# Kernel tuning notes

Hardware: AMD Instinct MI355X
Metric: run time of the kernel (lower is better)

Reference implementation:

```python
import jax, jax.numpy as jnp
import numpy as np

N = 262144
B = 16
C = 256
H = 8


def setup_inputs() -> dict:
    key = jax.random.key(0)
    ks = jax.random.split(key, 12)
    s = 0.02
    inp = {
        'x_a': jax.random.normal(ks[0], (N, C), jnp.float32),
        'x_b': jax.random.normal(ks[1], (N, C), jnp.float32),
        'offset': (jnp.arange(1, B + 1, dtype=jnp.int64) * (N // B)),
        'Wq': jax.random.normal(ks[2], (C, C), jnp.float32) * s,
        'Wk': jax.random.normal(ks[3], (C, C), jnp.float32) * s,
        'Wv': jax.random.normal(ks[4], (C, C), jnp.float32) * s,
        'Wp': jax.random.normal(ks[5], (C, C), jnp.float32) * s,
        'bp': jnp.zeros((C,), jnp.float32),
        'Wr1': jax.random.normal(ks[6], (C, C), jnp.float32) * s,
        'br1': jnp.zeros((C,), jnp.float32),
        'Wr2': jax.random.normal(ks[7], (C, C), jnp.float32) * s,
        'br2': jnp.zeros((C,), jnp.float32),
        'gamma': jnp.zeros((1,), jnp.float32),
        'Wo': jax.random.normal(ks[8], (C, C), jnp.float32) * s,
        'bo': jnp.zeros((C,), jnp.float32),
    }
    return inp


def reference(x_a, x_b, offset, Wq, Wk, Wv, Wp, bp, Wr1, br1, Wr2, br2, gamma, Wo, bo):
    n, c = x_a.shape
    b = offset.shape[0]
    h = H
    dh = c // h
    scale = dh ** -0.5
    # segment id for each point (offsets are cumulative counts)
    seg = jnp.searchsorted(offset, jnp.arange(n), side='right')
    counts = (offset - jnp.concatenate([jnp.zeros((1,), offset.dtype), offset[:-1]])).astype(x_a.dtype)
    # per-segment mean pool of branch A -> CLS queries
    cls_a = jax.ops.segment_sum(x_a, seg, num_segments=b) / counts[:, None]
    q = (cls_a @ Wq).reshape(b, h, dh)            # (B,H,Dh)
    k = (x_b @ Wk).reshape(n, h, dh)              # (N,H,Dh)
    v = (x_b @ Wv).reshape(n, h, dh)
    # ragged cross-attention: one query per segment over its own points
    logits = jnp.einsum('nhd,nhd->nh', k, q[seg]) * scale   # (N,H)
    m = jax.lax.stop_gradient(jax.ops.segment_max(logits, seg, num_segments=b))
    p = jnp.exp(logits - m[seg])
    denom = jax.ops.segment_sum(p, seg, num_segments=b)     # (B,H)
    w = p / denom[seg]
    out_cls = jax.ops.segment_sum(w[:, :, None] * v, seg, num_segments=b).reshape(b, c)
    out_cls = out_cls @ Wp + bp                   # proj (dropout = identity at eval)
    cls_proj = jax.nn.relu(out_cls @ Wr1 + br1) @ Wr2 + br2  # reproj MLP
    fused = x_a + gamma * cls_proj[seg]           # broadcast-scatter back to points
    return fused @ Wo + bo
```

## Files before the change

kernel.cpp:

```cpp
#include <hip/hip_runtime.h>


#define NPTS 262144
#define NSEG 16
#define CDIM 256
#define HNUM 8
#define DH   32
#define NB   2048

#define GEMM_BLOCKS 256
#define GEMM_NT     4096

using bf16x8 = __attribute__((ext_vector_type(8))) __bf16;
using f32x16 = __attribute__((ext_vector_type(16))) float;

__device__ __forceinline__ unsigned short f2bf(float f) {
  unsigned int u = __float_as_uint(f);
  unsigned int r = u + 0x7FFFu + ((u >> 16) & 1u);
  return (unsigned short)(r >> 16);
}

__device__ __forceinline__ bool off_is64(const int* o) { return o[1] == 0; }
__device__ __forceinline__ long long off_at(const int* o, int i, bool is64) {
  return is64 ? ((const long long*)o)[i] : (long long)o[i];
}
__device__ __forceinline__ int seg_of(long long row, const int* o, bool is64) {
  int s = 0;
  while (s < NSEG - 1 && row >= off_at(o, s, is64)) ++s;
  return s;
}

template <int CTRL>
__device__ __forceinline__ float dpp_add(float x) {
  int m = __builtin_amdgcn_update_dpp(0, __float_as_int(x), CTRL, 0xF, 0xF, true);
  return x + __int_as_float(m);
}

__device__ __forceinline__ void allred8(float lp[8]) {
  #pragma unroll
  for (int h = 0; h < 8; ++h) {
    float s = lp[h];
    s = dpp_add<0xB1>(s);
    s = dpp_add<0x4E>(s);
    s = dpp_add<0x124>(s);
    s = dpp_add<0x128>(s);
    s += __shfl_xor(s, 16, 64);
    s += __shfl_xor(s, 32, 64);
    lp[h] = s;
  }
}

__global__ __launch_bounds__(256) void k_wotseg(const float* __restrict__ Wo,
                                                unsigned short* __restrict__ wotp,
                                                const float* __restrict__ xa,
                                                const int* __restrict__ off,
                                                float* __restrict__ Apart,
                                                int* __restrict__ taga,
                                                float* __restrict__ cls_atomic,
                                                const float* __restrict__ gamma,
                                                int use_slots) {
  if (blockIdx.x < 256) {
    const int o = blockIdx.x * 256 + threadIdx.x;
    const int k = o >> 8, n = o & 255;
    wotp[n * CDIM + k] = f2bf(Wo[o]);
    return;
  }
  if (*gamma == 0.0f) return;
  const int bid = blockIdx.x - 256;
  const bool is64 = off_is64(off);
  const int t = threadIdx.x, lane = t & 63, w = t >> 6;
  const long long r0b = (long long)bid * 128;
  const int sg0 = seg_of(r0b, off, is64), sg1 = seg_of(r0b + 127, off, is64);
  const long long rw0 = r0b + (long long)w * 32;
  __shared__ float red[4][256];

  if (use_slots && sg0 == sg1) {
    float acc[4] = {0.f, 0.f, 0.f, 0.f};
    for (int r = 0; r < 32; ++r) {
      float4 xv = *(const float4*)&xa[(rw0 + r) * CDIM + lane * 4];
      acc[0] += xv.x; acc[1] += xv.y; acc[2] += xv.z; acc[3] += xv.w;
    }
    *(float4*)&red[w][lane * 4] = make_float4(acc[0], acc[1], acc[2], acc[3]);
    __syncthreads();
    Apart[bid * 256 + t] = red[0][t] + red[1][t] + red[2][t] + red[3][t];
    if (t == 0) taga[bid] = sg0;
  } else {
    int sg = seg_of(rw0, off, is64);
    long long segend = off_at(off, sg, is64);
    float acc[4] = {0.f, 0.f, 0.f, 0.f};
    for (int r = 0; r < 32; ++r) {
      long long row = rw0 + r;
      if (row >= segend) {
        #pragma unroll
        for (int i = 0; i < 4; ++i) { atomicAdd(&cls_atomic[sg * CDIM + lane * 4 + i], acc[i]); acc[i] = 0.f; }
        sg = seg_of(row, off, is64);
        segend = off_at(off, sg, is64);
      }
      float4 xv = *(const float4*)&xa[row * CDIM + lane * 4];
      acc[0] += xv.x; acc[1] += xv.y; acc[2] += xv.z; acc[3] += xv.w;
    }
    #pragma unroll
    for (int i = 0; i < 4; ++i) atomicAdd(&cls_atomic[sg * CDIM + lane * 4 + i], acc[i]);
    if (use_slots) {
      Apart[bid * 256 + t] = 0.f;
      if (t == 0) taga[bid] = -1;
    }
  }
}

__global__ __launch_bounds__(256) void k_prep(const float* __restrict__ Apart,
                                              const int* __restrict__ taga,
                                              const float* __restrict__ cls_atomic,
                                              const int* __restrict__ off,
                                              const float* __restrict__ Wq,
                                              const float* __restrict__ Wk,
                                              float* __restrict__ Kq,
                                              const float* __restrict__ gamma,
                                              int nb) {
  if (*gamma == 0.0f) return;
  const int b = blockIdx.x, t = threadIdx.x;
  const bool is64 = off_is64(off);
  __shared__ float cls[256], qv[256];
  long long lo = b ? off_at(off, b - 1, is64) : 0;
  long long hi = off_at(off, b, is64);
  float s = cls_atomic[b * CDIM + t];
  if (nb > 0) {
    int wlo = (int)(lo / 128); if (wlo < 0) wlo = 0;
    int whi = (int)((hi + 127) / 128); if (whi > nb) whi = nb;
    for (int w = wlo; w < whi; ++w)
      if (taga[w] == b) s += Apart[w * 256 + t];
  }
  cls[t] = s;
  __syncthreads();
  long long cnt = hi - lo; if (cnt < 1) cnt = 1;
  float inv = 1.0f / (float)cnt;
  float qs = 0.f;
  for (int c = 0; c < CDIM; ++c) qs += cls[c] * Wq[c * CDIM + t];
  qv[t] = qs * inv;
  __syncthreads();
  const float scale = 0.17677669529663687f;
  #pragma unroll
  for (int h = 0; h < HNUM; ++h) {
    float kk = 0.f;
    #pragma unroll 8
    for (int d = 0; d < DH; ++d) kk += Wk[t * CDIM + h * DH + d] * qv[h * DH + d];
    Kq[(b * HNUM + h) * CDIM + t] = kk * scale;
  }
}

__global__ __launch_bounds__(256) void k_stats(const float* __restrict__ xb,
                                               const int* __restrict__ off,
                                               const float* __restrict__ Kq,
                                               float* __restrict__ Spart,
                                               float* __restrict__ Dpart,
                                               int* __restrict__ tags,
                                               float* __restrict__ S_atomic,
                                               float* __restrict__ denom_atomic,
                                               const float* __restrict__ gamma,
                                               int use_slots) {
  if (*gamma == 0.0f) return;
  const bool is64 = off_is64(off);
  const int t = threadIdx.x, lane = t & 63, w = t >> 6;
  const long long r0b = (long long)blockIdx.x * 128;
  const int sg0 = seg_of(r0b, off, is64), sg1 = seg_of(r0b + 127, off, is64);
  const long long rw0 = r0b + (long long)w * 32;
  __shared__ float red[4][2048];
  __shared__ float dred[4][8];

  if (use_slots && sg0 == sg1) {
    float kq[8][4];
    #pragma unroll
    for (int h = 0; h < 8; ++h) {
      float4 v = *(const float4*)&Kq[(sg0 * 8 + h) * CDIM + lane * 4];
      kq[h][0] = v.x; kq[h][1] = v.y; kq[h][2] = v.z; kq[h][3] = v.w;
    }
    float sacc[8][4]; float dacc[8];
    #pragma unroll
    for (int h = 0; h < 8; ++h) { dacc[h] = 0.f; sacc[h][0]=sacc[h][1]=sacc[h][2]=sacc[h][3]=0.f; }

    #pragma unroll 2
    for (int r = 0; r < 32; ++r) {
      float4 xv = *(const float4*)&xb[(rw0 + r) * CDIM + lane * 4];
      float lp[8];
      #pragma unroll
      for (int h = 0; h < 8; ++h)
        lp[h] = xv.x*kq[h][0] + xv.y*kq[h][1] + xv.z*kq[h][2] + xv.w*kq[h][3];
      allred8(lp);
      #pragma unroll
      for (int h = 0; h < 8; ++h) {
        float p = __expf(lp[h]);
        dacc[h] += p;
        sacc[h][0] += p*xv.x; sacc[h][1] += p*xv.y; sacc[h][2] += p*xv.z; sacc[h][3] += p*xv.w;
      }
    }
    #pragma unroll
    for (int h = 0; h < 8; ++h)
      *(float4*)&red[w][h * 256 + lane * 4] = make_float4(sacc[h][0], sacc[h][1], sacc[h][2], sacc[h][3]);
    if (lane == 0) {
      #pragma unroll
      for (int h = 0; h < 8; ++h) dred[w][h] = dacc[h];
    }
    __syncthreads();
    #pragma unroll
    for (int k = 0; k < 8; ++k) {
      int e = k * 256 + t;
      Spart[(long long)blockIdx.x * 2048 + e] = red[0][e] + red[1][e] + red[2][e] + red[3][e];
    }
    if (t < 8) Dpart[blockIdx.x * 8 + t] = dred[0][t] + dred[1][t] + dred[2][t] + dred[3][t];
    if (t == 0) tags[blockIdx.x] = sg0;
  } else {
    int sg = seg_of(rw0, off, is64);
    long long segend = off_at(off, sg, is64);
    float kq[8][4];
    #pragma unroll
    for (int h = 0; h < 8; ++h) {
      float4 v = *(const float4*)&Kq[(sg * 8 + h) * CDIM + lane * 4];
      kq[h][0] = v.x; kq[h][1] = v.y; kq[h][2] = v.z; kq[h][3] = v.w;
    }
    float sacc[8][4]; float dacc[8];
    #pragma unroll
    for (int h = 0; h < 8; ++h) { dacc[h] = 0.f; sacc[h][0]=sacc[h][1]=sacc[h][2]=sacc[h][3]=0.f; }
    for (int r = 0; r < 32; ++r) {
      long long row = rw0 + r;
      if (row >= segend) {
        #pragma unroll
        for (int h = 0; h < 8; ++h) {
          #pragma unroll
          for (int i = 0; i < 4; ++i) { atomicAdd(&S_atomic[(sg*8+h)*CDIM + lane*4 + i], sacc[h][i]); sacc[h][i]=0.f; }
          if (lane == 0) atomicAdd(&denom_atomic[sg*8+h], dacc[h]);
          dacc[h] = 0.f;
        }
        sg = seg_of(row, off, is64);
        segend = off_at(off, sg, is64);
        #pragma unroll
        for (int h = 0; h < 8; ++h) {
          float4 v = *(const float4*)&Kq[(sg * 8 + h) * CDIM + lane * 4];
          kq[h][0] = v.x; kq[h][1] = v.y; kq[h][2] = v.z; kq[h][3] = v.w;
        }
      }
      float4 xv = *(const float4*)&xb[row * CDIM + lane * 4];
      float lp[8];
      #pragma unroll
      for (int h = 0; h < 8; ++h)
        lp[h] = xv.x*kq[h][0] + xv.y*kq[h][1] + xv.z*kq[h][2] + xv.w*kq[h][3];
      allred8(lp);
      #pragma unroll
      for (int h = 0; h < 8; ++h) {
        float p = __expf(lp[h]);
        dacc[h] += p;
        sacc[h][0] += p*xv.x; sacc[h][1] += p*xv.y; sacc[h][2] += p*xv.z; sacc[h][3] += p*xv.w;
      }
    }
    #pragma unroll
    for (int h = 0; h < 8; ++h) {
      #pragma unroll
      for (int i = 0; i < 4; ++i) atomicAdd(&S_atomic[(sg*8+h)*CDIM + lane*4 + i], sacc[h][i]);
      if (lane == 0) atomicAdd(&denom_atomic[sg*8+h], dacc[h]);
    }
    if (use_slots) {
      #pragma unroll
      for (int k = 0; k < 8; ++k) Spart[(long long)blockIdx.x * 2048 + k * 256 + t] = 0.f;
      if (t < 8) Dpart[blockIdx.x * 8 + t] = 0.f;
      if (t == 0) tags[blockIdx.x] = -1;
    }
  }
}

__global__ __launch_bounds__(256) void k_sred(const float* __restrict__ Spart,
                                              const float* __restrict__ Dpart,
                                              const int* __restrict__ tags,
                                              const float* __restrict__ S_atomic,
                                              const float* __restrict__ denom_atomic,
                                              const int* __restrict__ off,
                                              float* __restrict__ S,
                                              float* __restrict__ denom,
                                              const float* __restrict__ gamma,
                                              int nb) {
  if (*gamma == 0.0f) return;
  const int b = blockIdx.x >> 3, ch = blockIdx.x & 7, t = threadIdx.x;
  const bool is64 = off_is64(off);
  const int e = ch * 256 + t;
  long long lo = b ? off_at(off, b - 1, is64) : 0;
  long long hi = off_at(off, b, is64);
  int wlo = (int)(lo / 128); if (wlo < 0) wlo = 0;
  int whi = (int)((hi + 127) / 128); if (whi > nb) whi = nb;
  float s = S_atomic[b * 2048 + e];
  for (int w = wlo; w < whi; ++w)
    if (tags[w] == b) s += Spart[(long long)w * 2048 + e];
  S[b * 2048 + e] = s;
  if (ch == 0 && t < 8) {
    float d = denom_atomic[b * 8 + t];
    for (int w = wlo; w < whi; ++w)
      if (tags[w] == b) d += Dpart[w * 8 + t];
    denom[b * 8 + t] = d;
  }
}

__global__ __launch_bounds__(256) void k_post(const float* __restrict__ S,
                                              const float* __restrict__ denom,
                                              const float* __restrict__ Wv,
                                              const float* __restrict__ Wp, const float* __restrict__ bp,
                                              const float* __restrict__ Wr1, const float* __restrict__ br1,
                                              const float* __restrict__ Wr2, const float* __restrict__ br2,
                                              const float* __restrict__ gamma,
                                              const float* __restrict__ Wo, const float* __restrict__ bo,
                                              float* __restrict__ biasv) {
  const int b = blockIdx.x, t = threadIdx.x;
  const float g = *gamma;
  if (g == 0.0f) {
    biasv[b * CDIM + t] = bo[t];
    return;
  }
  __shared__ float sb[8][256];
  __shared__ float db[8];
  __shared__ float v0[256], v1[256];
  #pragma unroll
  for (int k = 0; k < 8; ++k) sb[k][t] = S[b * 2048 + k * 256 + t];
  if (t < 8) db[t] = denom[b * 8 + t];
  __syncthreads();
  const int h = t >> 5;
  float oc = 0.f;
  for (int c = 0; c < CDIM; ++c) oc += Wv[c * CDIM + t] * sb[h][c];
  oc /= db[h];
  v0[t] = oc;
  __syncthreads();
  float a = bp[t];
  for (int c = 0; c < CDIM; ++c) a += v0[c] * Wp[c * CDIM + t];
  v1[t] = a;
  __syncthreads();
  float r1 = br1[t];
  for (int c = 0; c < CDIM; ++c) r1 += v1[c] * Wr1[c * CDIM + t];
  r1 = fmaxf(r1, 0.f);
  v0[t] = r1;
  __syncthreads();
  float r2 = br2[t];
  for (int c = 0; c < CDIM; ++c) r2 += v0[c] * Wr2[c * CDIM + t];
  v1[t] = r2;
  __syncthreads();
  float acc = 0.f;
  for (int c = 0; c < CDIM; ++c) acc += v1[c] * Wo[c * CDIM + t];
  biasv[b * CDIM + t] = bo[t] + g * acc;
}

__device__ __forceinline__ void gemm_mfma_step(const unsigned short* Abuf,
                                               const unsigned short* Bs,
                                               int rA, int hi16, int nB0, int nB1, int sbyte,
                                               f32x16& acc0, f32x16& acc1) {
  #pragma unroll
  for (int ks = 0; ks < 4; ++ks) {
    const bf16x8 a = *(const bf16x8*)((const char*)Abuf + rA * 128 +
                       ((ks * 32 + hi16) ^ ((rA & 7) << 4)));
    const bf16x8 b0 = *(const bf16x8*)((const char*)Bs + nB0 * 512 +
                       ((sbyte + ks * 32 + hi16) ^ ((nB0 & 31) << 4)));
    const bf16x8 b1 = *(const bf16x8*)((const char*)Bs + nB1 * 512 +
                       ((sbyte + ks * 32 + hi16) ^ ((nB1 & 31) << 4)));
    acc0 = __builtin_amdgcn_mfma_f32_32x32x16_bf16(a, b0, acc0, 0, 0, 0);
    acc1 = __builtin_amdgcn_mfma_f32_32x32x16_bf16(a, b1, acc1, 0, 0, 0);
  }
}

__device__ __forceinline__ void gemm_cvt_write(const float4& sa, const float4& sb,
                                               unsigned short* Abuf, int aws0, int aws1) {
  unsigned int u0 = (unsigned int)f2bf(sa.x) | ((unsigned int)f2bf(sa.y) << 16);
  unsigned int u1 = (unsigned int)f2bf(sa.z) | ((unsigned int)f2bf(sa.w) << 16);
  unsigned int u2 = (unsigned int)f2bf(sb.x) | ((unsigned int)f2bf(sb.y) << 16);
  unsigned int u3 = (unsigned int)f2bf(sb.z) | ((unsigned int)f2bf(sb.w) << 16);
  uint2 w0; w0.x = u0; w0.y = u1;
  uint2 w1; w1.x = u2; w1.y = u3;
  *(uint2*)((char*)Abuf + aws0) = w0;
  *(uint2*)((char*)Abuf + aws1) = w1;
}

#define GEMM_BAR() do { asm volatile("s_waitcnt lgkmcnt(0)" ::: "memory"); \
                        __builtin_amdgcn_s_barrier(); } while (0)

#define GEMM_TILE(TCUR, PNEXT, c0,c1,c2,c3,c4,c5,c6,c7, n0,n1,n2,n3,n4,n5,n6,n7)   \
  {                                                                                 \
    f32x16 acc0 = {}, acc1 = {};                                                    \
    const long long r0 = (TCUR) * 64;                                               \
    gemm_cvt_write(c0, c1, As0, aws0, aws1);                                        \
    n0 = *(const float4*)(PNEXT);       n1 = *(const float4*)((PNEXT) + 32 * CDIM); \
    GEMM_BAR();                                                                     \
    gemm_mfma_step(As0, Bs, rA, hi16, nB0, nB1, 0, acc0, acc1);                     \
    gemm_cvt_write(c2, c3, As1, aws0, aws1);                                        \
    n2 = *(const float4*)((PNEXT) + 64); n3 = *(const float4*)((PNEXT) + 64 + 32 * CDIM); \
    GEMM_BAR();                                                                     \
    gemm_mfma_step(As1, Bs, rA, hi16, nB0, nB1, 128, acc0, acc1);                   \
    gemm_cvt_write(c4, c5, As0, aws0, aws1);                                        \
    n4 = *(const float4*)((PNEXT) + 128); n5 = *(const float4*)((PNEXT) + 128 + 32 * CDIM); \
    GEMM_BAR();                                                                     \
    gemm_mfma_step(As0, Bs, rA, hi16, nB0, nB1, 256, acc0, acc1);                   \
    gemm_cvt_write(c6, c7, As1, aws0, aws1);                                        \
    n6 = *(const float4*)((PNEXT) + 192); n7 = *(const float4*)((PNEXT) + 192 + 32 * CDIM); \
    GEMM_BAR();                                                                     \
    gemm_mfma_step(As1, Bs, rA, hi16, nB0, nB1, 384, acc0, acc1);                   \
    const int sg0 = seg_of(r0, off, is64);                                          \
    const bool uni = (sg0 == seg_of(r0 + 63, off, is64));                           \
    const int col0 = wx * 64 + (lane & 31);                                         \
    const int col1 = col0 + 32;                                                     \
    const float bvu0 = bias[sg0 * CDIM + col0];                                     \
    const float bvu1 = bias[sg0 * CDIM + col1];                                     \
    _Pragma("unroll")                                                               \
    for (int reg = 0; reg < 16; ++reg) {                                            \
      const int rin = wy * 32 + 4 * (lane >> 5) + (reg & 3) + 8 * (reg >> 2);       \
      const long long grow = r0 + rin;                                              \
      float bb0 = bvu0, bb1 = bvu1;                                                 \
      if (!uni) {                                                                   \
        const int sg = seg_of(grow, off, is64);                                     \
        bb0 = bias[sg * CDIM + col0];                                               \
        bb1 = bias[sg * CDIM + col1];                                               \
      }                                                                             \
      out[grow * CDIM + col0] = acc0[reg] + bb0;                                    \
      out[grow * CDIM + col1] = acc1[reg] + bb1;                                    \
    }                                                                               \
  }

__global__ __launch_bounds__(512, 2) void k_gemm(const float* __restrict__ xa,
                                                 const unsigned short* __restrict__ wot,
                                                 const float* __restrict__ bias,
                                                 const int* __restrict__ off,
                                                 float* __restrict__ out) {
  extern __shared__ char smem[];
  unsigned short* Bs  = (unsigned short*)smem;
  unsigned short* As0 = (unsigned short*)(smem + 131072);
  unsigned short* As1 = (unsigned short*)(smem + 131072 + 8192);

  const int t = threadIdx.x, lane = t & 63, w = t >> 6;
  const int wy = w >> 2, wx = w & 3;
  const bool is64 = off_is64(off);

  const int arow0 = t >> 4;
  const int ac = t & 15;
  const int arow1 = arow0 + 32;
  const int aws0 = arow0 * 128 + ((ac * 8) ^ ((arow0 & 7) << 4));
  const int aws1 = arow1 * 128 + ((ac * 8) ^ ((arow1 & 7) << 4));

  float4 a0, a1, a2, a3, a4, a5, a6, a7;
  float4 b0, b1, b2, b3, b4, b5, b6, b7;
  {
    const float* p = xa + ((long long)blockIdx.x * 64 + arow0) * CDIM + ac * 4;
    a0 = *(const float4*)(p);        a1 = *(const float4*)(p + 32 * CDIM);
    a2 = *(const float4*)(p + 64);   a3 = *(const float4*)(p + 64 + 32 * CDIM);
    a4 = *(const float4*)(p + 128);  a5 = *(const float4*)(p + 128 + 32 * CDIM);
    a6 = *(const float4*)(p + 192);  a7 = *(const float4*)(p + 192 + 32 * CDIM);
  }

  #pragma unroll
  for (int pp = 0; pp < 16; ++pp) {
    int q = t + pp * 512;
    int n = q >> 5, c = q & 31;
    uint4 u = *(const uint4*)(wot + n * CDIM + c * 8);
    int d = n * 512 + ((c * 16) ^ ((n & 31) << 4));
    *(uint4*)((char*)Bs + d) = u;
  }
  __syncthreads();

  const int rA = wy * 32 + (lane & 31);
  const int hi16 = (lane >> 5) * 16;
  const int nB0 = wx * 64 + (lane & 31);
  const int nB1 = nB0 + 32;

  long long tile = blockIdx.x;
  #pragma unroll 1
  for (int it = 0; it < 8; ++it) {
    const float* pn1 = xa + ((tile + GEMM_BLOCKS) * 64 + arow0) * CDIM + ac * 4;
    GEMM_TILE(tile, pn1, a0, a1, a2, a3, a4, a5, a6, a7,
                         b0, b1, b2, b3, b4, b5, b6, b7);
    const long long t2 = tile + 2 * GEMM_BLOCKS;
    const float* pn2 = xa + (((t2 < GEMM_NT) ? t2 : tile) * 64 + arow0) * CDIM + ac * 4;
    GEMM_TILE(tile + GEMM_BLOCKS, pn2, b0, b1, b2, b3, b4, b5, b6, b7,
                                       a0, a1, a2, a3, a4, a5, a6, a7);
    tile += 2 * GEMM_BLOCKS;
  }
}

extern "C" void kernel_launch(void* const* d_in, const int* in_sizes, int n_in,
                              void* d_out, int out_size, void* d_ws, size_t ws_size,
                              hipStream_t stream) {
  const float* xa    = (const float*)d_in[0];
  const float* xb    = (const float*)d_in[1];
  const int*   off   = (const int*)d_in[2];
  const float* Wq    = (const float*)d_in[3];
  const float* Wk    = (const float*)d_in[4];
  const float* Wv    = (const float*)d_in[5];
  const float* Wp    = (const float*)d_in[6];
  const float* bp    = (const float*)d_in[7];
  const float* Wr1   = (const float*)d_in[8];
  const float* br1   = (const float*)d_in[9];
  const float* Wr2   = (const float*)d_in[10];
  const float* br2   = (const float*)d_in[11];
  const float* gamma = (const float*)d_in[12];
  const float* Wo    = (const float*)d_in[13];
  const float* bo    = (const float*)d_in[14];
  float* out = (float*)d_out;

  float* ws = (float*)d_ws;
  float* S_atomic   = ws + 0;
  float* cls_atomic = ws + 32768;
  float* denom_at   = ws + 36864;
  float* S          = ws + 36992;
  float* denom      = ws + 69760;
  float* Kq         = ws + 69888;
  float* biasv      = ws + 102656;
  unsigned short* wot = (unsigned short*)(ws + 106752);
  int*   tags_s     = (int*)(ws + 139520);
  int*   taga       = (int*)(ws + 141568);
  float* Dpart      = ws + 143616;
  float* Apart      = ws + 160000;
  float* Spart      = ws + 684288;
  const size_t needed = (size_t)(684288 + 4194304) * 4;
  const int use_slots = (ws_size >= needed) ? 1 : 0;

  hipMemsetAsync(ws, 0, 36992 * sizeof(float), stream);

  k_wotseg<<<256 + NB, 256, 0, stream>>>(Wo, wot, xa, off, Apart, taga, cls_atomic, gamma, use_slots);
  k_prep  <<<16,   256, 0, stream>>>(Apart, taga, cls_atomic, off, Wq, Wk, Kq, gamma, use_slots ? NB : 0);
  k_stats <<<NB,   256, 0, stream>>>(xb, off, Kq, Spart, Dpart, tags_s, S_atomic, denom_at, gamma, use_slots);
  k_sred  <<<128,  256, 0, stream>>>(Spart, Dpart, tags_s, S_atomic, denom_at, off, S, denom, gamma, use_slots ? NB : 0);
  k_post  <<<16,   256, 0, stream>>>(S, denom, Wv, Wp, bp, Wr1, br1, Wr2, br2, gamma, Wo, bo, biasv);
  k_gemm  <<<GEMM_BLOCKS, 512, 147456, stream>>>(xa, wot, biasv, off, out);
}
```

Baseline: 128.5 us.

## Fold partial-sum reduction into post kernel and widen GEMM blocks to 1024 threads

Removes the separate k_sred launch by having k_post reduce the per-block slot partials directly into shared memory, which saves one kernel launch and a round trip through global memory. The output GEMM now uses 1024-thread blocks with 16 waves, each wave computing a single 32x32 tile. Previously 8 waves each computed a 32x64 tile with two accumulators. This halves per-thread register and prefetch state so more waves can hide memory latency, but it gives less MFMA work per B-fragment load. The fused reduction runs on only 16 blocks, which serializes work that k_sred spread across 128 blocks. With the default gamma of zero, that path exits early anyway.

```diff
diff --git a/kernel.cpp b/kernel.cpp
--- a/kernel.cpp
+++ b/kernel.cpp
@@ -266,57 +266,48 @@
   }
 }
 
-__global__ __launch_bounds__(256) void k_sred(const float* __restrict__ Spart,
+__global__ __launch_bounds__(256) void k_post(const float* __restrict__ Spart,
                                               const float* __restrict__ Dpart,
                                               const int* __restrict__ tags,
                                               const float* __restrict__ S_atomic,
                                               const float* __restrict__ denom_atomic,
                                               const int* __restrict__ off,
-                                              float* __restrict__ S,
-                                              float* __restrict__ denom,
-                                              const float* __restrict__ gamma,
-                                              int nb) {
-  if (*gamma == 0.0f) return;
-  const int b = blockIdx.x >> 3, ch = blockIdx.x & 7, t = threadIdx.x;
-  const bool is64 = off_is64(off);
-  const int e = ch * 256 + t;
-  long long lo = b ? off_at(off, b - 1, is64) : 0;
-  long long hi = off_at(off, b, is64);
-  int wlo = (int)(lo / 128); if (wlo < 0) wlo = 0;
-  int whi = (int)((hi + 127) / 128); if (whi > nb) whi = nb;
-  float s = S_atomic[b * 2048 + e];
-  for (int w = wlo; w < whi; ++w)
-    if (tags[w] == b) s += Spart[(long long)w * 2048 + e];
-  S[b * 2048 + e] = s;
-  if (ch == 0 && t < 8) {
-    float d = denom_atomic[b * 8 + t];
-    for (int w = wlo; w < whi; ++w)
-      if (tags[w] == b) d += Dpart[w * 8 + t];
-    denom[b * 8 + t] = d;
-  }
-}
-
-__global__ __launch_bounds__(256) void k_post(const float* __restrict__ S,
-                                              const float* __restrict__ denom,
                                               const float* __restrict__ Wv,
                                               const float* __restrict__ Wp, const float* __restrict__ bp,
                                               const float* __restrict__ Wr1, const float* __restrict__ br1,
                                               const float* __restrict__ Wr2, const float* __restrict__ br2,
                                               const float* __restrict__ gamma,
                                               const float* __restrict__ Wo, const float* __restrict__ bo,
-                                              float* __restrict__ biasv) {
+                                              float* __restrict__ biasv,
+                                              int nb) {
   const int b = blockIdx.x, t = threadIdx.x;
   const float g = *gamma;
   if (g == 0.0f) {
     biasv[b * CDIM + t] = bo[t];
     return;
   }
+  const bool is64 = off_is64(off);
   __shared__ float sb[8][256];
   __shared__ float db[8];
   __shared__ float v0[256], v1[256];
+  long long lo = b ? off_at(off, b - 1, is64) : 0;
+  long long hi = off_at(off, b, is64);
+  int wlo = (int)(lo / 128); if (wlo < 0) wlo = 0;
+  int whi = (int)((hi + 127) / 128); if (whi > nb) whi = nb;
   #pragma unroll
-  for (int k = 0; k < 8; ++k) sb[k][t] = S[b * 2048 + k * 256 + t];
-  if (t < 8) db[t] = denom[b * 8 + t];
+  for (int k = 0; k < 8; ++k) {
+    const int e = k * 256 + t;
+    float s = S_atomic[b * 2048 + e];
+    for (int w = wlo; w < whi; ++w)
+      if (tags[w] == b) s += Spart[(long long)w * 2048 + e];
+    sb[k][t] = s;
+  }
+  if (t < 8) {
+    float d = denom_atomic[b * 8 + t];
+    for (int w = wlo; w < whi; ++w)
+      if (tags[w] == b) d += Dpart[w * 8 + t];
+    db[t] = d;
+  }
   __syncthreads();
   const int h = t >> 5;
   float oc = 0.f;
@@ -342,112 +333,91 @@
   biasv[b * CDIM + t] = bo[t] + g * acc;
 }
 
-__device__ __forceinline__ void gemm_mfma_step(const unsigned short* Abuf,
-                                               const unsigned short* Bs,
-                                               int rA, int hi16, int nB0, int nB1, int sbyte,
-                                               f32x16& acc0, f32x16& acc1) {
-  #pragma unroll
-  for (int ks = 0; ks < 4; ++ks) {
-    const bf16x8 a = *(const bf16x8*)((const char*)Abuf + rA * 128 +
-                       ((ks * 32 + hi16) ^ ((rA & 7) << 4)));
-    const bf16x8 b0 = *(const bf16x8*)((const char*)Bs + nB0 * 512 +
-                       ((sbyte + ks * 32 + hi16) ^ ((nB0 & 31) << 4)));
-    const bf16x8 b1 = *(const bf16x8*)((const char*)Bs + nB1 * 512 +
-                       ((sbyte + ks * 32 + hi16) ^ ((nB1 & 31) << 4)));
-    acc0 = __builtin_amdgcn_mfma_f32_32x32x16_bf16(a, b0, acc0, 0, 0, 0);
-    acc1 = __builtin_amdgcn_mfma_f32_32x32x16_bf16(a, b1, acc1, 0, 0, 0);
-  }
-}
-
-__device__ __forceinline__ void gemm_cvt_write(const float4& sa, const float4& sb,
-                                               unsigned short* Abuf, int aws0, int aws1) {
-  unsigned int u0 = (unsigned int)f2bf(sa.x) | ((unsigned int)f2bf(sa.y) << 16);
-  unsigned int u1 = (unsigned int)f2bf(sa.z) | ((unsigned int)f2bf(sa.w) << 16);
-  unsigned int u2 = (unsigned int)f2bf(sb.x) | ((unsigned int)f2bf(sb.y) << 16);
-  unsigned int u3 = (unsigned int)f2bf(sb.z) | ((unsigned int)f2bf(sb.w) << 16);
-  uint2 w0; w0.x = u0; w0.y = u1;
-  uint2 w1; w1.x = u2; w1.y = u3;
-  *(uint2*)((char*)Abuf + aws0) = w0;
-  *(uint2*)((char*)Abuf + aws1) = w1;
+__device__ __forceinline__ void gemm_cvt1(const float4& s, unsigned short* Abuf, int aws) {
+  uint2 w;
+  w.x = (unsigned int)f2bf(s.x) | ((unsigned int)f2bf(s.y) << 16);
+  w.y = (unsigned int)f2bf(s.z) | ((unsigned int)f2bf(s.w) << 16);
+  *(uint2*)((char*)Abuf + aws) = w;
 }
 
 #define GEMM_BAR() do { asm volatile("s_waitcnt lgkmcnt(0)" ::: "memory"); \
                         __builtin_amdgcn_s_barrier(); } while (0)
 
-#define GEMM_TILE(TCUR, PNEXT, c0,c1,c2,c3,c4,c5,c6,c7, n0,n1,n2,n3,n4,n5,n6,n7)   \
+#define GEMM_PHASE(Abuf, sbyte)                                                     \
+  do {                                                                              \
+    _Pragma("unroll")                                                               \
+    for (int ks = 0; ks < 4; ++ks) {                                                \
+      const bf16x8 a = *(const bf16x8*)((const char*)(Abuf) + rA * 128 +            \
+                         ((ks * 32 + hi16) ^ ((rA & 7) << 4)));                     \
+      const bf16x8 b = *(const bf16x8*)((const char*)Bs + nB0 * 512 +               \
+                         (((sbyte) + ks * 32 + hi16) ^ ((nB0 & 31) << 4)));         \
+      acc = __builtin_amdgcn_mfma_f32_32x32x16_bf16(a, b, acc, 0, 0, 0);            \
+    }                                                                               \
+  } while (0)
+
+#define GEMM_TILE(TCUR, PNEXT, c0,c1,c2,c3, n0,n1,n2,n3)                            \
   {                                                                                 \
-    f32x16 acc0 = {}, acc1 = {};                                                    \
+    f32x16 acc = {};                                                                \
     const long long r0 = (TCUR) * 64;                                               \
-    gemm_cvt_write(c0, c1, As0, aws0, aws1);                                        \
-    n0 = *(const float4*)(PNEXT);       n1 = *(const float4*)((PNEXT) + 32 * CDIM); \
+    gemm_cvt1(c0, As0, aws);                                                        \
+    n0 = *(const float4*)(PNEXT);                                                   \
     GEMM_BAR();                                                                     \
-    gemm_mfma_step(As0, Bs, rA, hi16, nB0, nB1, 0, acc0, acc1);                     \
-    gemm_cvt_write(c2, c3, As1, aws0, aws1);                                        \
-    n2 = *(const float4*)((PNEXT) + 64); n3 = *(const float4*)((PNEXT) + 64 + 32 * CDIM); \
+    GEMM_PHASE(As0, 0);                                                             \
+    gemm_cvt1(c1, As1, aws);                                                        \
+    n1 = *(const float4*)((PNEXT) + 64);                                            \
     GEMM_BAR();                                                                     \
-    gemm_mfma_step(As1, Bs, rA, hi16, nB0, nB1, 128, acc0, acc1);                   \
-    gemm_cvt_write(c4, c5, As0, aws0, aws1);                                        \
-    n4 = *(const float4*)((PNEXT) + 128); n5 = *(const float4*)((PNEXT) + 128 + 32 * CDIM); \
+    GEMM_PHASE(As1, 128);                                                           \
+    gemm_cvt1(c2, As0, aws);                                                        \
+    n2 = *(const float4*)((PNEXT) + 128);                                           \
     GEMM_BAR();                                                                     \
-    gemm_mfma_step(As0, Bs, rA, hi16, nB0, nB1, 256, acc0, acc1);                   \
-    gemm_cvt_write(c6, c7, As1, aws0, aws1);                                        \
-    n6 = *(const float4*)((PNEXT) + 192); n7 = *(const float4*)((PNEXT) + 192 + 32 * CDIM); \
+    GEMM_PHASE(As0, 256);                                                           \
+    gemm_cvt1(c3, As1, aws);                                                        \
+    n3 = *(const float4*)((PNEXT) + 192);                                           \
     GEMM_BAR();                                                                     \
-    gemm_mfma_step(As1, Bs, rA, hi16, nB0, nB1, 384, acc0, acc1);                   \
+    GEMM_PHASE(As1, 384);                                                           \
     const int sg0 = seg_of(r0, off, is64);                                          \
     const bool uni = (sg0 == seg_of(r0 + 63, off, is64));                           \
-    const int col0 = wx * 64 + (lane & 31);                                         \
-    const int col1 = col0 + 32;                                                     \
-    const float bvu0 = bias[sg0 * CDIM + col0];                                     \
-    const float bvu1 = bias[sg0 * CDIM + col1];                                     \
+    const float bvu = bias[sg0 * CDIM + col0];                                      \
     _Pragma("unroll")                                                               \
     for (int reg = 0; reg < 16; ++reg) {                                            \
       const int rin = wy * 32 + 4 * (lane >> 5) + (reg & 3) + 8 * (reg >> 2);       \
       const long long grow = r0 + rin;                                              \
-      float bb0 = bvu0, bb1 = bvu1;                                                 \
-      if (!uni) {                                                                   \
-        const int sg = seg_of(grow, off, is64);                                     \
-        bb0 = bias[sg * CDIM + col0];                                               \
-        bb1 = bias[sg * CDIM + col1];                                               \
-      }                                                                             \
-      out[grow * CDIM + col0] = acc0[reg] + bb0;                                    \
-      out[grow * CDIM + col1] = acc1[reg] + bb1;                                    \
+      float bb = uni ? bvu : bias[seg_of(grow, off, is64) * CDIM + col0];           \
+      out[grow * CDIM + col0] = acc[reg] + bb;                                      \
     }                                                                               \
   }
 
-__global__ __launch_bounds__(512, 2) void k_gemm(const float* __restrict__ xa,
-                                                 const unsigned short* __restrict__ wot,
-                                                 const float* __restrict__ bias,
-                                                 const int* __restrict__ off,
-                                                 float* __restrict__ out) {
+__global__ __launch_bounds__(1024, 4) void k_gemm(const float* __restrict__ xa,
+                                                  const unsigned short* __restrict__ wot,
+                                                  const float* __restrict__ bias,
+                                                  const int* __restrict__ off,
+                                                  float* __restrict__ out) {
   extern __shared__ char smem[];
   unsigned short* Bs  = (unsigned short*)smem;
   unsigned short* As0 = (unsigned short*)(smem + 131072);
   unsigned short* As1 = (unsigned short*)(smem + 131072 + 8192);
 
   const int t = threadIdx.x, lane = t & 63, w = t >> 6;
-  const int wy = w >> 2, wx = w & 3;
+  const int wy = w >> 3, wx = w & 7;
   const bool is64 = off_is64(off);
 
-  const int arow0 = t >> 4;
+  const int arow = t >> 4;
   const int ac = t & 15;
-  const int arow1 = arow0 + 32;
-  const int aws0 = arow0 * 128 + ((ac * 8) ^ ((arow0 & 7) << 4));
-  const int aws1 = arow1 * 128 + ((ac * 8) ^ ((arow1 & 7) << 4));
-
-  float4 a0, a1, a2, a3, a4, a5, a6, a7;
-  float4 b0, b1, b2, b3, b4, b5, b6, b7;
+  const int aws = arow * 128 + ((ac * 8) ^ ((arow & 7) << 4));
+
+  float4 a0, a1, a2, a3;
+  float4 b0, b1, b2, b3;
   {
-    const float* p = xa + ((long long)blockIdx.x * 64 + arow0) * CDIM + ac * 4;
-    a0 = *(const float4*)(p);        a1 = *(const float4*)(p + 32 * CDIM);
-    a2 = *(const float4*)(p + 64);   a3 = *(const float4*)(p + 64 + 32 * CDIM);
-    a4 = *(const float4*)(p + 128);  a5 = *(const float4*)(p + 128 + 32 * CDIM);
-    a6 = *(const float4*)(p + 192);  a7 = *(const float4*)(p + 192 + 32 * CDIM);
+    const float* p = xa + ((long long)blockIdx.x * 64 + arow) * CDIM + ac * 4;
+    a0 = *(const float4*)(p);
+    a1 = *(const float4*)(p + 64);
+    a2 = *(const float4*)(p + 128);
+    a3 = *(const float4*)(p + 192);
   }
 
   #pragma unroll
-  for (int pp = 0; pp < 16; ++pp) {
-    int q = t + pp * 512;
+  for (int pp = 0; pp < 8; ++pp) {
+    int q = t + pp * 1024;
     int n = q >> 5, c = q & 31;
     uint4 u = *(const uint4*)(wot + n * CDIM + c * 8);
     int d = n * 512 + ((c * 16) ^ ((n & 31) << 4));
@@ -457,19 +427,17 @@
 
   const int rA = wy * 32 + (lane & 31);
   const int hi16 = (lane >> 5) * 16;
-  const int nB0 = wx * 64 + (lane & 31);
-  const int nB1 = nB0 + 32;
+  const int nB0 = wx * 32 + (lane & 31);
+  const int col0 = wx * 32 + (lane & 31);
 
   long long tile = blockIdx.x;
   #pragma unroll 1
   for (int it = 0; it < 8; ++it) {
-    const float* pn1 = xa + ((tile + GEMM_BLOCKS) * 64 + arow0) * CDIM + ac * 4;
-    GEMM_TILE(tile, pn1, a0, a1, a2, a3, a4, a5, a6, a7,
-                         b0, b1, b2, b3, b4, b5, b6, b7);
+    const float* pn1 = xa + ((tile + GEMM_BLOCKS) * 64 + arow) * CDIM + ac * 4;
+    GEMM_TILE(tile, pn1, a0, a1, a2, a3, b0, b1, b2, b3);
     const long long t2 = tile + 2 * GEMM_BLOCKS;
-    const float* pn2 = xa + (((t2 < GEMM_NT) ? t2 : tile) * 64 + arow0) * CDIM + ac * 4;
-    GEMM_TILE(tile + GEMM_BLOCKS, pn2, b0, b1, b2, b3, b4, b5, b6, b7,
-                                       a0, a1, a2, a3, a4, a5, a6, a7);
+    const float* pn2 = xa + (((t2 < GEMM_NT) ? t2 : tile) * 64 + arow) * CDIM + ac * 4;
+    GEMM_TILE(tile + GEMM_BLOCKS, pn2, b0, b1, b2, b3, a0, a1, a2, a3);
     tile += 2 * GEMM_BLOCKS;
   }
 }
@@ -498,8 +466,6 @@
   float* S_atomic   = ws + 0;
   float* cls_atomic = ws + 32768;
   float* denom_at   = ws + 36864;
-  float* S          = ws + 36992;
-  float* denom      = ws + 69760;
   float* Kq         = ws + 69888;
   float* biasv      = ws + 102656;
   unsigned short* wot = (unsigned short*)(ws + 106752);
@@ -516,7 +482,7 @@
   k_wotseg<<<256 + NB, 256, 0, stream>>>(Wo, wot, xa, off, Apart, taga, cls_atomic, gamma, use_slots);
   k_prep  <<<16,   256, 0, stream>>>(Apart, taga, cls_atomic, off, Wq, Wk, Kq, gamma, use_slots ? NB : 0);
   k_stats <<<NB,   256, 0, stream>>>(xb, off, Kq, Spart, Dpart, tags_s, S_atomic, denom_at, gamma, use_slots);
-  k_sred  <<<128,  256, 0, stream>>>(Spart, Dpart, tags_s, S_atomic, denom_at, off, S, denom, gamma, use_slots ? NB : 0);
-  k_post  <<<16,   256, 0, stream>>>(S, denom, Wv, Wp, bp, Wr1, br1, Wr2, br2, gamma, Wo, bo, biasv);
-  k_gemm  <<<GEMM_BLOCKS, 512, 147456, stream>>>(xa, wot, biasv, off, out);
-}
+  k_post  <<<16,   256, 0, stream>>>(Spart, Dpart, tags_s, S_atomic, denom_at, off, Wv, Wp, bp,
+                                     Wr1, br1, Wr2, br2, gamma, Wo, bo, biasv, use_slots ? NB : 0);
+  k_gemm  <<<GEMM_BLOCKS, 1024, 147456, stream>>>(xa, wot, biasv, off, out);
+}
```

Measured after the change: 130.9 us. Within noise of the previous version (+1.9%).

## Fuse Wo transpose into GEMM, merge S reduction into post, nontemporal stores

Applied to the files above, without the earlier changes.

Drops the separate Wo bf16 transpose blocks and has each GEMM block convert and transpose Wo straight into shared memory. The k_sred reduction kernel is folded into k_post, and the GEMM reads bo directly when gamma is zero, so the bias prep can be skipped. Output stores become nontemporal. The aim is fewer launches and less workspace traffic, at the cost of every GEMM block redoing the Wo conversion and k_post's 16 blocks serially reducing the partials.

```diff
diff --git a/kernel.cpp b/kernel.cpp
--- a/kernel.cpp
+++ b/kernel.cpp
@@ -50,26 +50,17 @@
   }
 }
 
-__global__ __launch_bounds__(256) void k_wotseg(const float* __restrict__ Wo,
-                                                unsigned short* __restrict__ wotp,
-                                                const float* __restrict__ xa,
+__global__ __launch_bounds__(256) void k_segsum(const float* __restrict__ xa,
                                                 const int* __restrict__ off,
                                                 float* __restrict__ Apart,
                                                 int* __restrict__ taga,
                                                 float* __restrict__ cls_atomic,
                                                 const float* __restrict__ gamma,
                                                 int use_slots) {
-  if (blockIdx.x < 256) {
-    const int o = blockIdx.x * 256 + threadIdx.x;
-    const int k = o >> 8, n = o & 255;
-    wotp[n * CDIM + k] = f2bf(Wo[o]);
-    return;
-  }
   if (*gamma == 0.0f) return;
-  const int bid = blockIdx.x - 256;
   const bool is64 = off_is64(off);
   const int t = threadIdx.x, lane = t & 63, w = t >> 6;
-  const long long r0b = (long long)bid * 128;
+  const long long r0b = (long long)blockIdx.x * 128;
   const int sg0 = seg_of(r0b, off, is64), sg1 = seg_of(r0b + 127, off, is64);
   const long long rw0 = r0b + (long long)w * 32;
   __shared__ float red[4][256];
@@ -82,8 +73,8 @@
     }
     *(float4*)&red[w][lane * 4] = make_float4(acc[0], acc[1], acc[2], acc[3]);
     __syncthreads();
-    Apart[bid * 256 + t] = red[0][t] + red[1][t] + red[2][t] + red[3][t];
-    if (t == 0) taga[bid] = sg0;
+    Apart[blockIdx.x * 256 + t] = red[0][t] + red[1][t] + red[2][t] + red[3][t];
+    if (t == 0) taga[blockIdx.x] = sg0;
   } else {
     int sg = seg_of(rw0, off, is64);
     long long segend = off_at(off, sg, is64);
@@ -102,8 +93,8 @@
     #pragma unroll
     for (int i = 0; i < 4; ++i) atomicAdd(&cls_atomic[sg * CDIM + lane * 4 + i], acc[i]);
     if (use_slots) {
-      Apart[bid * 256 + t] = 0.f;
-      if (t == 0) taga[bid] = -1;
+      Apart[blockIdx.x * 256 + t] = 0.f;
+      if (t == 0) taga[blockIdx.x] = -1;
     }
   }
 }
@@ -266,57 +257,45 @@
   }
 }
 
-__global__ __launch_bounds__(256) void k_sred(const float* __restrict__ Spart,
+__global__ __launch_bounds__(256) void k_post(const float* __restrict__ Spart,
                                               const float* __restrict__ Dpart,
                                               const int* __restrict__ tags,
                                               const float* __restrict__ S_atomic,
                                               const float* __restrict__ denom_atomic,
                                               const int* __restrict__ off,
-                                              float* __restrict__ S,
-                                              float* __restrict__ denom,
-                                              const float* __restrict__ gamma,
-                                              int nb) {
-  if (*gamma == 0.0f) return;
-  const int b = blockIdx.x >> 3, ch = blockIdx.x & 7, t = threadIdx.x;
-  const bool is64 = off_is64(off);
-  const int e = ch * 256 + t;
-  long long lo = b ? off_at(off, b - 1, is64) : 0;
-  long long hi = off_at(off, b, is64);
-  int wlo = (int)(lo / 128); if (wlo < 0) wlo = 0;
-  int whi = (int)((hi + 127) / 128); if (whi > nb) whi = nb;
-  float s = S_atomic[b * 2048 + e];
-  for (int w = wlo; w < whi; ++w)
-    if (tags[w] == b) s += Spart[(long long)w * 2048 + e];
-  S[b * 2048 + e] = s;
-  if (ch == 0 && t < 8) {
-    float d = denom_atomic[b * 8 + t];
-    for (int w = wlo; w < whi; ++w)
-      if (tags[w] == b) d += Dpart[w * 8 + t];
-    denom[b * 8 + t] = d;
-  }
-}
-
-__global__ __launch_bounds__(256) void k_post(const float* __restrict__ S,
-                                              const float* __restrict__ denom,
                                               const float* __restrict__ Wv,
                                               const float* __restrict__ Wp, const float* __restrict__ bp,
                                               const float* __restrict__ Wr1, const float* __restrict__ br1,
                                               const float* __restrict__ Wr2, const float* __restrict__ br2,
                                               const float* __restrict__ gamma,
                                               const float* __restrict__ Wo, const float* __restrict__ bo,
-                                              float* __restrict__ biasv) {
+                                              float* __restrict__ biasv,
+                                              int nb) {
   const int b = blockIdx.x, t = threadIdx.x;
   const float g = *gamma;
-  if (g == 0.0f) {
-    biasv[b * CDIM + t] = bo[t];
-    return;
-  }
+  if (g == 0.0f) return;
+  const bool is64 = off_is64(off);
   __shared__ float sb[8][256];
   __shared__ float db[8];
   __shared__ float v0[256], v1[256];
+  long long lo = b ? off_at(off, b - 1, is64) : 0;
+  long long hi = off_at(off, b, is64);
+  int wlo = (int)(lo / 128); if (wlo < 0) wlo = 0;
+  int whi = (int)((hi + 127) / 128); if (whi > nb) whi = nb;
   #pragma unroll
-  for (int k = 0; k < 8; ++k) sb[k][t] = S[b * 2048 + k * 256 + t];
-  if (t < 8) db[t] = denom[b * 8 + t];
+  for (int k = 0; k < 8; ++k) {
+    const int e = k * 256 + t;
+    float s = S_atomic[b * 2048 + e];
+    for (int w = wlo; w < whi; ++w)
+      if (tags[w] == b) s += Spart[(long long)w * 2048 + e];
+    sb[k][t] = s;
+  }
+  if (t < 8) {
+    float d = denom_atomic[b * 8 + t];
+    for (int w = wlo; w < whi; ++w)
+      if (tags[w] == b) d += Dpart[w * 8 + t];
+    db[t] = d;
+  }
   __syncthreads();
   const int h = t >> 5;
   float oc = 0.f;
@@ -395,11 +374,12 @@
     GEMM_BAR();                                                                     \
     gemm_mfma_step(As1, Bs, rA, hi16, nB0, nB1, 384, acc0, acc1);                   \
     const int sg0 = seg_of(r0, off, is64);                                          \
-    const bool uni = (sg0 == seg_of(r0 + 63, off, is64));                           \
+    const bool uni = g0 || (sg0 == seg_of(r0 + 63, off, is64));                     \
+    const float* bsrc = g0 ? bo : (bias + sg0 * CDIM);                              \
     const int col0 = wx * 64 + (lane & 31);                                         \
     const int col1 = col0 + 32;                                                     \
-    const float bvu0 = bias[sg0 * CDIM + col0];                                     \
-    const float bvu1 = bias[sg0 * CDIM + col1];                                     \
+    const float bvu0 = bsrc[col0];                                                  \
+    const float bvu1 = bsrc[col1];                                                  \
     _Pragma("unroll")                                                               \
     for (int reg = 0; reg < 16; ++reg) {                                            \
       const int rin = wy * 32 + 4 * (lane >> 5) + (reg & 3) + 8 * (reg >> 2);       \
@@ -410,14 +390,16 @@
         bb0 = bias[sg * CDIM + col0];                                               \
         bb1 = bias[sg * CDIM + col1];                                               \
       }                                                                             \
-      out[grow * CDIM + col0] = acc0[reg] + bb0;                                    \
-      out[grow * CDIM + col1] = acc1[reg] + bb1;                                    \
+      __builtin_nontemporal_store(acc0[reg] + bb0, &out[grow * CDIM + col0]);       \
+      __builtin_nontemporal_store(acc1[reg] + bb1, &out[grow * CDIM + col1]);       \
     }                                                                               \
   }
 
 __global__ __launch_bounds__(512, 2) void k_gemm(const float* __restrict__ xa,
-                                                 const unsigned short* __restrict__ wot,
+                                                 const float* __restrict__ Wo,
                                                  const float* __restrict__ bias,
+                                                 const float* __restrict__ bo,
+                                                 const float* __restrict__ gamma,
                                                  const int* __restrict__ off,
                                                  float* __restrict__ out) {
   extern __shared__ char smem[];
@@ -428,6 +410,7 @@
   const int t = threadIdx.x, lane = t & 63, w = t >> 6;
   const int wy = w >> 2, wx = w & 3;
   const bool is64 = off_is64(off);
+  const bool g0 = (*gamma == 0.0f);
 
   const int arow0 = t >> 4;
   const int ac = t & 15;
@@ -445,13 +428,30 @@
     a6 = *(const float4*)(p + 192);  a7 = *(const float4*)(p + 192 + 32 * CDIM);
   }
 
-  #pragma unroll
-  for (int pp = 0; pp < 16; ++pp) {
-    int q = t + pp * 512;
-    int n = q >> 5, c = q & 31;
-    uint4 u = *(const uint4*)(wot + n * CDIM + c * 8);
-    int d = n * 512 + ((c * 16) ^ ((n & 31) << 4));
-    *(uint4*)((char*)Bs + d) = u;
+  {
+    const int tn0 = (t & 63) * 4;
+    const int tk0 = (t >> 6) * 4;
+    #pragma unroll
+    for (int i = 0; i < 8; ++i) {
+      const int k0 = tk0 + i * 32;
+      float4 r0v = *(const float4*)&Wo[(k0 + 0) * CDIM + tn0];
+      float4 r1v = *(const float4*)&Wo[(k0 + 1) * CDIM + tn0];
+      float4 r2v = *(const float4*)&Wo[(k0 + 2) * CDIM + tn0];
+      float4 r3v = *(const float4*)&Wo[(k0 + 3) * CDIM + tn0];
+      const float* f0 = (const float*)&r0v;
+      const float* f1 = (const float*)&r1v;
+      const float* f2 = (const float*)&r2v;
+      const float* f3 = (const float*)&r3v;
+      #pragma unroll
+      for (int j = 0; j < 4; ++j) {
+        const int n = tn0 + j;
+        uint2 wv;
+        wv.x = (unsigned int)f2bf(f0[j]) | ((unsigned int)f2bf(f1[j]) << 16);
+        wv.y = (unsigned int)f2bf(f2[j]) | ((unsigned int)f2bf(f3[j]) << 16);
+        const int d = n * 512 + ((2 * k0) ^ ((n & 31) << 4));
+        *(uint2*)((char*)Bs + d) = wv;
+      }
+    }
   }
   __syncthreads();
 
@@ -498,11 +498,8 @@
   float* S_atomic   = ws + 0;
   float* cls_atomic = ws + 32768;
   float* denom_at   = ws + 36864;
-  float* S          = ws + 36992;
-  float* denom      = ws + 69760;
   float* Kq         = ws + 69888;
   float* biasv      = ws + 102656;
-  unsigned short* wot = (unsigned short*)(ws + 106752);
   int*   tags_s     = (int*)(ws + 139520);
   int*   taga       = (int*)(ws + 141568);
   float* Dpart      = ws + 143616;
@@ -513,10 +510,10 @@
 
   hipMemsetAsync(ws, 0, 36992 * sizeof(float), stream);
 
-  k_wotseg<<<256 + NB, 256, 0, stream>>>(Wo, wot, xa, off, Apart, taga, cls_atomic, gamma, use_slots);
-  k_prep  <<<16,   256, 0, stream>>>(Apart, taga, cls_atomic, off, Wq, Wk, Kq, gamma, use_slots ? NB : 0);
-  k_stats <<<NB,   256, 0, stream>>>(xb, off, Kq, Spart, Dpart, tags_s, S_atomic, denom_at, gamma, use_slots);
-  k_sred  <<<128,  256, 0, stream>>>(Spart, Dpart, tags_s, S_atomic, denom_at, off, S, denom, gamma, use_slots ? NB : 0);
-  k_post  <<<16,   256, 0, stream>>>(S, denom, Wv, Wp, bp, Wr1, br1, Wr2, br2, gamma, Wo, bo, biasv);
-  k_gemm  <<<GEMM_BLOCKS, 512, 147456, stream>>>(xa, wot, biasv, off, out);
-}
+  k_segsum<<<NB,  256, 0, stream>>>(xa, off, Apart, taga, cls_atomic, gamma, use_slots);
+  k_prep  <<<16,  256, 0, stream>>>(Apart, taga, cls_atomic, off, Wq, Wk, Kq, gamma, use_slots ? NB : 0);
+  k_stats <<<NB,  256, 0, stream>>>(xb, off, Kq, Spart, Dpart, tags_s, S_atomic, denom_at, gamma, use_slots);
+  k_post  <<<16,  256, 0, stream>>>(Spart, Dpart, tags_s, S_atomic, denom_at, off, Wv, Wp, bp,
+                                    Wr1, br1, Wr2, br2, gamma, Wo, bo, biasv, use_slots ? NB : 0);
+  k_gemm  <<<GEMM_BLOCKS, 512, 147456, stream>>>(xa, Wo, biasv, bo, gamma, off, out);
+}
```

Result: faster. 107.8 us (-16.1%).
